# Kernel optimization log

Measured on AMD Instinct MI355X. Metric: run time of the kernel, lower is better.

Reference implementation:

```python
import jax, jax.numpy as jnp
import numpy as np

B, N, K, C = 4, 4096, 32, 192  # batch, npoint, nsample, channels (C % 6 == 0)
EPS = 1e-5


def setup_inputs() -> dict:
    key = jax.random.key(0)
    ks = jax.random.split(key, 8)
    p = jax.random.normal(ks[0], (B, N, 3), jnp.float32)
    x = jax.random.normal(ks[1], (B, C, N), jnp.float32)
    idx = jax.random.randint(ks[2], (B, N, K), 0, N)  # ball-query neighbor ids
    W = jax.random.normal(ks[3], (C, C + 3), jnp.float32) * 0.05  # 1x1 conv weight
    gamma = 1.0 + 0.1 * jax.random.normal(ks[4], (C,), jnp.float32)
    beta = 0.1 * jax.random.normal(ks[5], (C,), jnp.float32)
    rmean = 0.1 * jax.random.normal(ks[6], (C,), jnp.float32)
    rvar = jax.random.uniform(ks[7], (C,), jnp.float32) + 0.5  # positive running var
    return dict(p=p, x=x, idx=idx, W=W, gamma=gamma, beta=beta, rmean=rmean, rvar=rvar)


def reference(p, x, idx, W, gamma, beta, rmean, rvar):
    # --- grouper: gather neighbors, relative coords ---
    pn = jax.vmap(lambda pp, ii: pp[ii])(p, idx)            # [B,N,K,3]
    dp = jnp.transpose(pn - p[:, :, None, :], (0, 3, 1, 2))  # [B,3,N,K]
    xj = jax.vmap(lambda xx, ii: xx[:, ii])(x, idx)          # [B,C,N,K]
    # --- PosPool sin/cos positional embedding fused with features ---
    feat_dim = C // 6
    dim_mat = jnp.power(500.0, jnp.arange(feat_dim, dtype=jnp.float32) / feat_dim)
    div = (50.0 * dp)[..., None] / dim_mat                   # [B,3,N,K,fd]
    pe = jnp.concatenate([jnp.sin(div), jnp.cos(div)], axis=-1)  # [B,3,N,K,2fd]
    pe = jnp.transpose(pe, (0, 1, 4, 2, 3)).reshape(B, C, N, K)  # [B,C,N,K]
    agg = xj * pe + pe
    # --- dp_fj concat -> 1x1 conv -> BN(eval) -> ReLU ---
    h = jnp.concatenate([dp, agg], axis=1)                   # [B,C+3,N,K]
    y = jnp.einsum('oc,bcnk->bonk', W, h)                    # [B,C,N,K]
    inv = gamma / jnp.sqrt(rvar + EPS)
    y = y * inv[:, None, None] + (beta - rmean * inv)[:, None, None]
    y = jax.nn.relu(y)
    # --- max reduction over neighbors ---
    return jnp.max(y, axis=-1)                               # [B,C,N]
```

## Files before the change

kernel.cpp:

```cpp
#include <hip/hip_runtime.h>
#include <math.h>

#define B_   4
#define N_   4096
#define K_   32
#define C_   192
#define CH_  195
#define KPAD 224
#define NKT6 6
#define NNT  4
#define GRID 768

using half8  = __attribute__((ext_vector_type(8))) _Float16;
using half2v = __attribute__((ext_vector_type(2))) _Float16;
using f32x4  = __attribute__((ext_vector_type(4))) float;

__device__ _Float16 g_Wp[C_ * KPAD];
__device__ _Float16 g_xT[(size_t)B_ * N_ * C_];

__global__ __launch_bounds__(256) void prep(const float* __restrict__ x,
                                            const float* __restrict__ W,
                                            const float* __restrict__ gamma_,
                                            const float* __restrict__ rvar) {
    const int tid = threadIdx.x;
    if (blockIdx.x < 512) {
        __shared__ float s[32][201];
        const int b  = blockIdx.x >> 7;
        const int n0 = (blockIdx.x & 127) * 32;
        const int cl = tid >> 3;
        const int n4 = (tid & 7) * 4;
#pragma unroll
        for (int it = 0; it < 6; ++it) {
            const int c = it * 32 + cl;
            const float4 v = *(const float4*)(x + ((size_t)b * C_ + c) * N_ + n0 + n4);
            s[n4 + 0][c] = v.x; s[n4 + 1][c] = v.y; s[n4 + 2][c] = v.z; s[n4 + 3][c] = v.w;
        }
        __syncthreads();
        const int n  = tid >> 3;
        const int og = tid & 7;
#pragma unroll
        for (int it = 0; it < 3; ++it) {
            const int oc = it * 8 + og;
            half8 v;
#pragma unroll
            for (int jj = 0; jj < 8; ++jj) v[jj] = (_Float16)s[n][oc * 8 + jj];
            *(half8*)(g_xT + ((size_t)b * N_ + n0 + n) * C_ + oc * 8) = v;
        }
    } else {
        const int i = (blockIdx.x - 512) * 256 + tid;
        if (i < C_ * KPAD) {
            const int o = i / KPAD, r = i - o * KPAD;
            const float inv = gamma_[o] * rsqrtf(rvar[o] + 1e-5f);
            float v = 0.0f;
            if (r < 192)      v = W[o * CH_ + 3 + r];
            else if (r < 195) v = W[o * CH_ + (r - 192)];
            g_Wp[i] = (_Float16)(v * inv);
        }
    }
}

__global__ __launch_bounds__(256, 3) void la_mfma(
    const float* __restrict__ p,
    const int*   __restrict__ idx,
    const float* __restrict__ gamma_,
    const float* __restrict__ beta_,
    const float* __restrict__ rmean,
    const float* __restrict__ rvar,
    float* __restrict__ out)
{
    __shared__ _Float16 hb[2][NKT6 * NNT * 64 * 8];
    __shared__ float s_d[2][3][64];
    __shared__ float s_bias[C_], s_fr[32];

    const int tid  = threadIdx.x;
    const int lane = tid & 63;
    const int w    = tid >> 6;
    const int l15  = lane & 15;
    const int quad = lane >> 4;

    const int xcd    = blockIdx.x & 7;
    const int slot   = blockIdx.x >> 3;
    const int st     = (slot < 64) ? slot * 11 : slot * 10 + 64;
    const int npairs = (slot < 64) ? 11 : 10;
    const int pair0  = xcd * 1024 + st;
    const int b      = xcd >> 1;

    if (tid < C_) {
        const float inv = gamma_[tid] * rsqrtf(rvar[tid] + 1e-5f);
        s_bias[tid] = beta_[tid] - rmean[tid] * inv;
    }
    if (tid < 32) s_fr[tid] = 7.9577471546f * exp2f(-(float)tid * 0.2801808715263400f);
    __syncthreads();

    float sfr[8];
#pragma unroll
    for (int jj = 0; jj < 8; ++jj) sfr[jj] = s_fr[quad * 8 + jj];

    const int pt = w >> 1;
    const int k  = (w & 1) * 16 + l15;

    int j = idx[(size_t)(pair0 * 2 + pt) * K_ + k];

    for (int it = 0; it < npairs; ++it) {
        const int cur = it & 1;
        const int bn0 = (pair0 + it) * 2;
        const int n0  = bn0 & (N_ - 1);
        const int gp  = bn0 + pt;

        const float d0 = p[(size_t)(b * N_ + j) * 3 + 0] - p[(size_t)gp * 3 + 0];
        const float d1 = p[(size_t)(b * N_ + j) * 3 + 1] - p[(size_t)gp * 3 + 1];
        const float d2 = p[(size_t)(b * N_ + j) * 3 + 2] - p[(size_t)gp * 3 + 2];
        const _Float16* xh = g_xT + ((size_t)b * N_ + j) * C_;

#pragma unroll
        for (int i6 = 0; i6 < 6; ++i6) {
            const int chunk = quad + 4 * i6;
            const half8 v = *(const half8*)(xh + chunk * 8);
            const float dd  = (chunk < 8) ? d0 : ((chunk < 16) ? d1 : d2);
            const float off = (chunk & 4) ? 0.25f : 0.0f;
            half8 hv;
#pragma unroll
            for (int jj = 0; jj < 8; jj += 2) {
                const float pe0 = __builtin_amdgcn_sinf(fmaf(dd, sfr[jj],     off));
                const float pe1 = __builtin_amdgcn_sinf(fmaf(dd, sfr[jj + 1], off));
                const half2v pe2 = __builtin_bit_cast(half2v, __builtin_amdgcn_cvt_pkrtz(pe0, pe1));
                half2v v2; v2[0] = v[jj]; v2[1] = v[jj + 1];
                const half2v r2 = pe2 * v2 + pe2;
                hv[jj] = r2[0]; hv[jj + 1] = r2[1];
            }
            *(half8*)(&hb[cur][(size_t)((i6 * NNT + w) * 64 + quad * 16 + l15) * 8]) = hv;
        }
        if (quad == 0) {
            const int col = w * 16 + l15;
            s_d[cur][0][col] = d0; s_d[cur][1][col] = d1; s_d[cur][2][col] = d2;
        }
        __syncthreads();

        {
            const int itn = (it + 1 < npairs) ? it + 1 : it;
            j = idx[(size_t)((pair0 + itn) * 2 + pt) * K_ + k];
        }

        f32x4 acc[3][4];
#pragma unroll
        for (int i = 0; i < 3; ++i)
#pragma unroll
            for (int t = 0; t < 4; ++t) acc[i][t] = (f32x4)0.0f;

#pragma unroll
        for (int kt = 0; kt < NKT6; ++kt) {
            const int k0 = kt * 32 + quad * 8;
            half8 a[3], bf[4];
#pragma unroll
            for (int i = 0; i < 3; ++i)
                a[i] = *(const half8*)(g_Wp + (size_t)((w * 3 + i) * 16 + l15) * KPAD + k0);
#pragma unroll
            for (int t = 0; t < 4; ++t)
                bf[t] = *(const half8*)(&hb[cur][(size_t)((kt * NNT + t) * 64 + lane) * 8]);
#pragma unroll
            for (int i = 0; i < 3; ++i)
#pragma unroll
                for (int t = 0; t < 4; ++t)
                    acc[i][t] = __builtin_amdgcn_mfma_f32_16x16x32_f16(bf[t], a[i], acc[i][t], 0, 0, 0);
        }
        {
            half8 a6[3];
#pragma unroll
            for (int i = 0; i < 3; ++i)
                a6[i] = *(const half8*)(g_Wp + (size_t)((w * 3 + i) * 16 + l15) * KPAD + 6 * 32 + quad * 8);
#pragma unroll
            for (int t = 0; t < 4; ++t) {
                const int col = t * 16 + l15;
                half8 b6 = (half8)(_Float16)0.0f;
                const float e0 = s_d[cur][0][col];
                const float e1 = s_d[cur][1][col];
                const float e2 = s_d[cur][2][col];
                if (quad == 0) {
                    b6[0] = (_Float16)e0; b6[1] = (_Float16)e1; b6[2] = (_Float16)e2;
                }
#pragma unroll
                for (int i = 0; i < 3; ++i)
                    acc[i][t] = __builtin_amdgcn_mfma_f32_16x16x32_f16(b6, a6[i], acc[i][t], 0, 0, 0);
            }
        }

#pragma unroll
        for (int i = 0; i < 3; ++i) {
            const int m = (w * 3 + i) * 16 + l15;
            float vv[2];
#pragma unroll
            for (int ptc = 0; ptc < 2; ++ptc) {
                const f32x4 va = acc[i][2 * ptc];
                const f32x4 vb = acc[i][2 * ptc + 1];
                float v = fmaxf(fmaxf(fmaxf(va[0], va[1]), fmaxf(va[2], va[3])),
                                fmaxf(fmaxf(vb[0], vb[1]), fmaxf(vb[2], vb[3])));
                v = fmaxf(v, __shfl_xor(v, 16, 64));
                v = fmaxf(v, __shfl_xor(v, 32, 64));
                vv[ptc] = v;
            }
            if (quad == 0) {
                const float bias = s_bias[m];
                float2 o2;
                o2.x = fmaxf(vv[0] + bias, 0.0f);
                o2.y = fmaxf(vv[1] + bias, 0.0f);
                *(float2*)(&out[((size_t)b * C_ + m) * N_ + n0]) = o2;
            }
        }
    }
}

extern "C" void kernel_launch(void* const* d_in, const int* in_sizes, int n_in,
                              void* d_out, int out_size, void* d_ws, size_t ws_size,
                              hipStream_t stream) {
    (void)in_sizes; (void)n_in; (void)out_size; (void)d_ws; (void)ws_size;
    const float* p      = (const float*)d_in[0];
    const float* x      = (const float*)d_in[1];
    const int*   idx    = (const int*)d_in[2];
    const float* W      = (const float*)d_in[3];
    const float* gamma_ = (const float*)d_in[4];
    const float* beta_  = (const float*)d_in[5];
    const float* rmean  = (const float*)d_in[6];
    const float* rvar   = (const float*)d_in[7];
    float* out = (float*)d_out;

    prep<<<512 + (C_ * KPAD + 255) / 256, 256, 0, stream>>>(x, W, gamma_, rvar);
    la_mfma<<<GRID, 256, 0, stream>>>(p, idx, gamma_, beta_, rmean, rvar, out);
}
```

Measured before the change: 158.4 us.

## Process two point-pairs per iteration to widen MFMA tile and reuse weights

Result: slower. 170.3 us (+7.5%).

```diff
diff --git a/kernel.cpp b/kernel.cpp
--- a/kernel.cpp
+++ b/kernel.cpp
@@ -8,7 +8,7 @@
 #define CH_  195
 #define KPAD 224
 #define NKT6 6
-#define NNT  4
+#define NNT8 8
 #define GRID 768
 
 using half8  = __attribute__((ext_vector_type(8))) _Float16;
@@ -68,8 +68,8 @@
     const float* __restrict__ rvar,
     float* __restrict__ out)
 {
-    __shared__ _Float16 hb[2][NKT6 * NNT * 64 * 8];
-    __shared__ float s_d[2][3][64];
+    __shared__ _Float16 hb[NKT6 * NNT8 * 64 * 8];
+    __shared__ float s_d[3][128];
     __shared__ float s_bias[C_], s_fr[32];
 
     const int tid  = threadIdx.x;
@@ -80,9 +80,9 @@
 
     const int xcd    = blockIdx.x & 7;
     const int slot   = blockIdx.x >> 3;
-    const int st     = (slot < 64) ? slot * 11 : slot * 10 + 64;
-    const int npairs = (slot < 64) ? 11 : 10;
-    const int pair0  = xcd * 1024 + st;
+    const int iters  = (slot < 32) ? 6 : 5;
+    const int pstart = (slot < 32) ? slot * 12 : 384 + (slot - 32) * 10;
+    const int pairbase = xcd * 1024 + pstart;
     const int b      = xcd >> 1;
 
     if (tid < C_) {
@@ -99,69 +99,73 @@
     const int pt = w >> 1;
     const int k  = (w & 1) * 16 + l15;
 
-    int j = idx[(size_t)(pair0 * 2 + pt) * K_ + k];
-
-    for (int it = 0; it < npairs; ++it) {
-        const int cur = it & 1;
-        const int bn0 = (pair0 + it) * 2;
-        const int n0  = bn0 & (N_ - 1);
-        const int gp  = bn0 + pt;
-
-        const float d0 = p[(size_t)(b * N_ + j) * 3 + 0] - p[(size_t)gp * 3 + 0];
-        const float d1 = p[(size_t)(b * N_ + j) * 3 + 1] - p[(size_t)gp * 3 + 1];
-        const float d2 = p[(size_t)(b * N_ + j) * 3 + 2] - p[(size_t)gp * 3 + 2];
-        const _Float16* xh = g_xT + ((size_t)b * N_ + j) * C_;
-
-#pragma unroll
-        for (int i6 = 0; i6 < 6; ++i6) {
-            const int chunk = quad + 4 * i6;
-            const half8 v = *(const half8*)(xh + chunk * 8);
-            const float dd  = (chunk < 8) ? d0 : ((chunk < 16) ? d1 : d2);
-            const float off = (chunk & 4) ? 0.25f : 0.0f;
-            half8 hv;
-#pragma unroll
-            for (int jj = 0; jj < 8; jj += 2) {
-                const float pe0 = __builtin_amdgcn_sinf(fmaf(dd, sfr[jj],     off));
-                const float pe1 = __builtin_amdgcn_sinf(fmaf(dd, sfr[jj + 1], off));
-                const half2v pe2 = __builtin_bit_cast(half2v, __builtin_amdgcn_cvt_pkrtz(pe0, pe1));
-                half2v v2; v2[0] = v[jj]; v2[1] = v[jj + 1];
-                const half2v r2 = pe2 * v2 + pe2;
-                hv[jj] = r2[0]; hv[jj + 1] = r2[1];
-            }
-            *(half8*)(&hb[cur][(size_t)((i6 * NNT + w) * 64 + quad * 16 + l15) * 8]) = hv;
-        }
-        if (quad == 0) {
-            const int col = w * 16 + l15;
-            s_d[cur][0][col] = d0; s_d[cur][1][col] = d1; s_d[cur][2][col] = d2;
+    int j0 = idx[(size_t)((pairbase + 0) * 2 + pt) * K_ + k];
+    int j1 = idx[(size_t)((pairbase + 1) * 2 + pt) * K_ + k];
+
+    for (int it = 0; it < iters; ++it) {
+        const int pr0 = pairbase + 2 * it;
+        const int n0  = (pr0 * 2) & (N_ - 1);
+
+#pragma unroll
+        for (int pp = 0; pp < 2; ++pp) {
+            const int j  = pp ? j1 : j0;
+            const int gp = (pr0 + pp) * 2 + pt;
+            const float d0 = p[(size_t)(b * N_ + j) * 3 + 0] - p[(size_t)gp * 3 + 0];
+            const float d1 = p[(size_t)(b * N_ + j) * 3 + 1] - p[(size_t)gp * 3 + 1];
+            const float d2 = p[(size_t)(b * N_ + j) * 3 + 2] - p[(size_t)gp * 3 + 2];
+            const _Float16* xh = g_xT + ((size_t)b * N_ + j) * C_;
+            const int nt = pp * 4 + w;
+
+#pragma unroll
+            for (int i6 = 0; i6 < 6; ++i6) {
+                const int chunk = quad + 4 * i6;
+                const half8 v = *(const half8*)(xh + chunk * 8);
+                const float dd  = (chunk < 8) ? d0 : ((chunk < 16) ? d1 : d2);
+                const float off = (chunk & 4) ? 0.25f : 0.0f;
+                half8 hv;
+#pragma unroll
+                for (int jj = 0; jj < 8; jj += 2) {
+                    const float pe0 = __builtin_amdgcn_sinf(fmaf(dd, sfr[jj],     off));
+                    const float pe1 = __builtin_amdgcn_sinf(fmaf(dd, sfr[jj + 1], off));
+                    const half2v pe2 = __builtin_bit_cast(half2v, __builtin_amdgcn_cvt_pkrtz(pe0, pe1));
+                    half2v v2; v2[0] = v[jj]; v2[1] = v[jj + 1];
+                    const half2v r2 = pe2 * v2 + pe2;
+                    hv[jj] = r2[0]; hv[jj + 1] = r2[1];
+                }
+                *(half8*)(&hb[(size_t)((i6 * NNT8 + nt) * 64 + quad * 16 + l15) * 8]) = hv;
+            }
+            if (quad == 0) {
+                const int col = nt * 16 + l15;
+                s_d[0][col] = d0; s_d[1][col] = d1; s_d[2][col] = d2;
+            }
         }
         __syncthreads();
 
-        {
-            const int itn = (it + 1 < npairs) ? it + 1 : it;
-            j = idx[(size_t)((pair0 + itn) * 2 + pt) * K_ + k];
-        }
-
-        f32x4 acc[3][4];
+        if (it + 1 < iters) {
+            j0 = idx[(size_t)((pr0 + 2) * 2 + pt) * K_ + k];
+            j1 = idx[(size_t)((pr0 + 3) * 2 + pt) * K_ + k];
+        }
+
+        f32x4 acc[3][8];
 #pragma unroll
         for (int i = 0; i < 3; ++i)
 #pragma unroll
-            for (int t = 0; t < 4; ++t) acc[i][t] = (f32x4)0.0f;
+            for (int t = 0; t < 8; ++t) acc[i][t] = (f32x4)0.0f;
 
 #pragma unroll
         for (int kt = 0; kt < NKT6; ++kt) {
             const int k0 = kt * 32 + quad * 8;
-            half8 a[3], bf[4];
+            half8 a[3];
 #pragma unroll
             for (int i = 0; i < 3; ++i)
                 a[i] = *(const half8*)(g_Wp + (size_t)((w * 3 + i) * 16 + l15) * KPAD + k0);
 #pragma unroll
-            for (int t = 0; t < 4; ++t)
-                bf[t] = *(const half8*)(&hb[cur][(size_t)((kt * NNT + t) * 64 + lane) * 8]);
-#pragma unroll
-            for (int i = 0; i < 3; ++i)
-#pragma unroll
-                for (int t = 0; t < 4; ++t)
-                    acc[i][t] = __builtin_amdgcn_mfma_f32_16x16x32_f16(bf[t], a[i], acc[i][t], 0, 0, 0);
+            for (int t = 0; t < 8; ++t) {
+                const half8 bf = *(const half8*)(&hb[(size_t)((kt * NNT8 + t) * 64 + lane) * 8]);
+#pragma unroll
+                for (int i = 0; i < 3; ++i)
+                    acc[i][t] = __builtin_amdgcn_mfma_f32_16x16x32_f16(bf, a[i], acc[i][t], 0, 0, 0);
+            }
         }
         {
             half8 a6[3];
@@ -169,12 +173,12 @@
             for (int i = 0; i < 3; ++i)
                 a6[i] = *(const half8*)(g_Wp + (size_t)((w * 3 + i) * 16 + l15) * KPAD + 6 * 32 + quad * 8);
 #pragma unroll
-            for (int t = 0; t < 4; ++t) {
+            for (int t = 0; t < 8; ++t) {
                 const int col = t * 16 + l15;
                 half8 b6 = (half8)(_Float16)0.0f;
-                const float e0 = s_d[cur][0][col];
-                const float e1 = s_d[cur][1][col];
-                const float e2 = s_d[cur][2][col];
+                const float e0 = s_d[0][col];
+                const float e1 = s_d[1][col];
+                const float e2 = s_d[2][col];
                 if (quad == 0) {
                     b6[0] = (_Float16)e0; b6[1] = (_Float16)e1; b6[2] = (_Float16)e2;
                 }
@@ -187,25 +191,30 @@
 #pragma unroll
         for (int i = 0; i < 3; ++i) {
             const int m = (w * 3 + i) * 16 + l15;
-            float vv[2];
-#pragma unroll
-            for (int ptc = 0; ptc < 2; ++ptc) {
-                const f32x4 va = acc[i][2 * ptc];
-                const f32x4 vb = acc[i][2 * ptc + 1];
-                float v = fmaxf(fmaxf(fmaxf(va[0], va[1]), fmaxf(va[2], va[3])),
-                                fmaxf(fmaxf(vb[0], vb[1]), fmaxf(vb[2], vb[3])));
-                v = fmaxf(v, __shfl_xor(v, 16, 64));
-                v = fmaxf(v, __shfl_xor(v, 32, 64));
-                vv[ptc] = v;
-            }
+            float4 o4;
+            float ov[4];
+#pragma unroll
+            for (int pp = 0; pp < 2; ++pp)
+#pragma unroll
+                for (int ptc = 0; ptc < 2; ++ptc) {
+                    const f32x4 va = acc[i][pp * 4 + 2 * ptc];
+                    const f32x4 vb = acc[i][pp * 4 + 2 * ptc + 1];
+                    float v = fmaxf(fmaxf(fmaxf(va[0], va[1]), fmaxf(va[2], va[3])),
+                                    fmaxf(fmaxf(vb[0], vb[1]), fmaxf(vb[2], vb[3])));
+                    v = fmaxf(v, __shfl_xor(v, 16, 64));
+                    v = fmaxf(v, __shfl_xor(v, 32, 64));
+                    ov[pp * 2 + ptc] = v;
+                }
             if (quad == 0) {
                 const float bias = s_bias[m];
-                float2 o2;
-                o2.x = fmaxf(vv[0] + bias, 0.0f);
-                o2.y = fmaxf(vv[1] + bias, 0.0f);
-                *(float2*)(&out[((size_t)b * C_ + m) * N_ + n0]) = o2;
-            }
-        }
+                o4.x = fmaxf(ov[0] + bias, 0.0f);
+                o4.y = fmaxf(ov[1] + bias, 0.0f);
+                o4.z = fmaxf(ov[2] + bias, 0.0f);
+                o4.w = fmaxf(ov[3] + bias, 0.0f);
+                *(float4*)(&out[((size_t)b * C_ + m) * N_ + n0]) = o4;
+            }
+        }
+        __syncthreads();
     }
 }
 
```
